# Optimization experiments

Hardware: AMD Instinct MI355X
Metric: run time of the kernel (lower is better)

Reference implementation:

```python
import jax, jax.numpy as jnp
import numpy as np

NUM_HEADS = 16
EMBED_DIM = 1024
HEAD_DIM = EMBED_DIM // NUM_HEADS  # 64


def setup_inputs() -> dict:
    key = jax.random.key(0)
    k1, k2, k3 = jax.random.split(key, 3)
    x = jax.random.normal(k1, (2, 2048, EMBED_DIM), dtype=jnp.float32)
    # torch Linear(head_dim, 3*head_dim): weight [3*hd, hd], bias [3*hd]
    # stored here as W_qkv [hd, 3*hd] so that y = x @ W_qkv + b
    lim = 1.0 / np.sqrt(HEAD_DIM)
    W_qkv = jax.random.uniform(k2, (HEAD_DIM, 3 * HEAD_DIM), minval=-lim, maxval=lim, dtype=jnp.float32)
    b_qkv = jax.random.uniform(k3, (3 * HEAD_DIM,), minval=-lim, maxval=lim, dtype=jnp.float32)
    return {"x": x, "W_qkv": W_qkv, "b_qkv": b_qkv}


def reference(x, W_qkv, b_qkv):
    B, T, E = x.shape
    # [B, T, E] -> [B, H, T, hd]
    xh = x.reshape(B, T, NUM_HEADS, HEAD_DIM).transpose(0, 2, 1, 3)
    qkv = xh @ W_qkv + b_qkv  # [B, H, T, 3*hd], shared weights across heads
    q, k, v = jnp.split(qkv, 3, axis=-1)
    scale = 1.0 / jnp.sqrt(jnp.asarray(HEAD_DIM, dtype=x.dtype))
    scores = jnp.einsum('bhqd,bhkd->bhqk', q, k) * scale  # [B, H, T, T]
    attn = jax.nn.softmax(scores, axis=-1)
    out = jnp.einsum('bhqk,bhkd->bhqd', attn, v)  # [B, H, T, hd]
    return out.transpose(0, 2, 1, 3).reshape(B, T, E)
```

## Files before the change

### kernel.cpp

```cpp
#include <hip/hip_runtime.h>
#include <hip/hip_bf16.h>

#define T_SEQ   2048
#define EMBED   1024
#define HD      64
#define NHEADS  16
#define NBH     32
#define QSCALE  0.18033688011112042f

typedef __attribute__((ext_vector_type(8))) short short8;
typedef __attribute__((ext_vector_type(4))) float f32x4;
typedef __attribute__((ext_vector_type(16))) float f32x16;
typedef __attribute__((ext_vector_type(2))) unsigned int uint2v;
typedef __attribute__((ext_vector_type(4))) unsigned int uint4v;

#if __has_builtin(__builtin_amdgcn_exp2f)
#define EXP2F __builtin_amdgcn_exp2f
#else
#define EXP2F exp2f
#endif

__device__ __forceinline__ ushort bf16r(float f) {
  union { float f; unsigned u; } v; v.f = f;
  return (ushort)((v.u + 0x8000u) >> 16);
}

__device__ __forceinline__ unsigned pk2bf_perm(float a, float b) {
  union { float f; unsigned u; } ua, ub; ua.f = a; ub.f = b;
  return __builtin_amdgcn_perm(ub.u + 0x8000u, ua.u + 0x8000u, 0x07060302u);
}
#if __has_builtin(__builtin_amdgcn_cvt_pk_bf16_f32)
typedef __attribute__((ext_vector_type(2))) __bf16 bf16x2;
__device__ __forceinline__ unsigned pkbf(float a, float b) {
  union { bf16x2 v; unsigned u; } c;
  c.v = __builtin_amdgcn_cvt_pk_bf16_f32(a, b);
  return c.u;
}
#else
#define pkbf pk2bf_perm
#endif

__device__ __forceinline__ uint2v pl32swap(unsigned a, unsigned b) {
#if __has_builtin(__builtin_amdgcn_permlane32_swap)
  return __builtin_amdgcn_permlane32_swap(a, b, false, false);
#else
  asm("v_permlane32_swap_b32 %0, %1" : "+v"(a), "+v"(b));
  return (uint2v){a, b};
#endif
}

__device__ __forceinline__ void async16(const ushort* g, ushort* l) {
  __builtin_amdgcn_global_load_lds(
      (const __attribute__((address_space(1))) unsigned int*)g,
      (__attribute__((address_space(3))) unsigned int*)l, 16, 0, 0);
}

__global__ __launch_bounds__(256) void prep_w(const float* __restrict__ W,
                                              ushort* __restrict__ Wg) {
  const int i = blockIdx.x * 256 + threadIdx.x;
  const int d = i / 192, c = i - d * 192;
  const int phys = c * 64 + (((d >> 3) ^ (c & 7)) << 3) + (d & 7);
  Wg[phys] = bf16r(W[i]);
}

__global__ __launch_bounds__(256) void qkv_proj(
    const float* __restrict__ x, const ushort* __restrict__ Wg,
    const float* __restrict__ bias,
    ushort* __restrict__ Qws, ushort* __restrict__ Kws,
    ushort* __restrict__ Vtws) {
  __shared__ ushort WtL[192 * 64];
  __shared__ __attribute__((aligned(16))) float bl[192];

  const int bx = blockIdx.x;
  const int b  = bx >> 9;
  const int h  = (bx >> 5) & 15;
  const int t0 = (bx & 31) * 64;
  const int tid = threadIdx.x;
  const int wave = tid >> 6, lane = tid & 63;
  const int quad = lane >> 4, n16 = lane & 15;

  const int trow = t0 + wave * 16 + n16;
  const float* xr = x + ((size_t)(b * T_SEQ + trow)) * EMBED + h * HD;
  short8 xa[2];
#pragma unroll
  for (int ks = 0; ks < 2; ks++) {
    f32x4 v0 = *(const f32x4*)(xr + ks * 32 + quad * 8);
    f32x4 v1 = *(const f32x4*)(xr + ks * 32 + quad * 8 + 4);
    short8 f;
    ((unsigned*)&f)[0] = pkbf(v0[0], v0[1]);
    ((unsigned*)&f)[1] = pkbf(v0[2], v0[3]);
    ((unsigned*)&f)[2] = pkbf(v1[0], v1[1]);
    ((unsigned*)&f)[3] = pkbf(v1[2], v1[3]);
    xa[ks] = f;
  }

#pragma unroll
  for (int it = 0; it < 6; it++)
    async16(Wg + it * 2048 + tid * 8, WtL + it * 2048 + wave * 512);
  if (tid < 192) bl[tid] = bias[tid];
  __syncthreads();

  const int bh = b * NHEADS + h;
  const size_t qkbase = (size_t)bh * T_SEQ * HD;
  const int tw = t0 + wave * 16;
  const int sw = n16 & 7;
  const int t = tw + n16;

#pragma unroll
  for (int nt = 0; nt < 12; nt++) {
    const ushort* wrow = WtL + (nt * 16 + n16) * 64;
    const short8 wb0 = *(short8*)(wrow + ((quad ^ sw) << 3));
    const short8 wb1 = *(short8*)(wrow + (((4 | quad) ^ sw) << 3));
    if (nt < 8) {
      f32x4 acc = (f32x4){0.f, 0.f, 0.f, 0.f};
      acc = __builtin_amdgcn_mfma_f32_16x16x32_bf16(wb0, xa[0], acc, 0, 0, 0);
      acc = __builtin_amdgcn_mfma_f32_16x16x32_bf16(wb1, xa[1], acc, 0, 0, 0);
      const f32x4 bv4 = *(const f32x4*)(bl + nt * 16 + quad * 4);
      uint2v pk;
      if (nt < 4) {
        const int d = nt * 16 + quad * 4;
        pk.x = pkbf((acc[0] + bv4[0]) * QSCALE, (acc[1] + bv4[1]) * QSCALE);
        pk.y = pkbf((acc[2] + bv4[2]) * QSCALE, (acc[3] + bv4[3]) * QSCALE);
        *(uint2v*)(Qws + qkbase + (size_t)t * HD + d) = pk;
      } else {
        const int d = (nt - 4) * 16 + quad * 4;
        pk.x = pkbf(acc[0] + bv4[0], acc[1] + bv4[1]);
        pk.y = pkbf(acc[2] + bv4[2], acc[3] + bv4[3]);
        *(uint2v*)(Kws + qkbase + (size_t)t * HD + d) = pk;
      }
    } else {
      f32x4 acc = (f32x4){0.f, 0.f, 0.f, 0.f};
      acc = __builtin_amdgcn_mfma_f32_16x16x32_bf16(xa[0], wb0, acc, 0, 0, 0);
      acc = __builtin_amdgcn_mfma_f32_16x16x32_bf16(xa[1], wb1, acc, 0, 0, 0);
      const float bv = bl[nt * 16 + n16];
      const int d = (nt - 8) * 16 + n16;
      const int tcol = tw + quad * 4;
      uint2v pk;
      pk.x = pkbf(acc[0] + bv, acc[1] + bv);
      pk.y = pkbf(acc[2] + bv, acc[3] + bv);
      *(uint2v*)(Vtws + (size_t)(bh * HD + d) * T_SEQ + tcol) = pk;
    }
  }
}

__global__ __launch_bounds__(256, 2) void flash_attn(
    const ushort* __restrict__ Qws, const ushort* __restrict__ Kws,
    const ushort* __restrict__ Vtws, float* __restrict__ out) {
  __shared__ ushort Ks[4][64 * 64];
  __shared__ ushort Vs[4][64 * 64];

  const int bx = blockIdx.x;
  const int bh = bx & 31;
  const int q0 = (bx >> 5) * 128;
  const int b = bh >> 4, h = bh & 15;
  const int tid = threadIdx.x;
  const int wave = tid >> 6, lane = tid & 63;
  const int l5 = lane & 31, H = lane >> 5, swz = lane & 7;

  const ushort* Qb = Qws + (size_t)bh * T_SEQ * HD;
  const ushort* Kb = Kws + (size_t)bh * T_SEQ * HD;
  const ushort* Vb = Vtws + (size_t)bh * HD * T_SEQ;

  short8 qb[4];
#pragma unroll
  for (int dc = 0; dc < 4; dc++)
    qb[dc] = *(const short8*)(Qb + (size_t)(q0 + wave * 32 + l5) * HD +
                              dc * 16 + H * 8);

  const int sr = tid >> 3, sp = tid & 7;
  const int sl = (sp ^ (sr & 7) ^ (((sr >> 4) & 1) << 1)) * 8;
  const ushort* pK0 = Kb + (size_t)sr * HD + sl;
  const ushort* pK1 = Kb + (size_t)(sr + 32) * HD + sl;
  const ushort* pV0 = Vb + (size_t)sr * T_SEQ + sl;
  const ushort* pV1 = Vb + (size_t)(sr + 32) * T_SEQ + sl;

  const int xr4 = ((l5 >> 4) & 1) << 1;
  int co[4];
#pragma unroll
  for (int i = 0; i < 4; i++) co[i] = ((((i << 1) | H) ^ swz ^ xr4) << 3);
  const int rbase = l5 << 6;

  short8 ones;
#pragma unroll
  for (int j = 0; j < 8; j++) ones[j] = (short)0x3F80;

  f32x16 o0, o1, lA;
#pragma unroll
  for (int i = 0; i < 16; i++) { o0[i] = 0.f; o1[i] = 0.f; lA[i] = 0.f; }

  async16(pK0, Ks[0] + wave * 512);
  async16(pK1, Ks[0] + 2048 + wave * 512);
  async16(pV0, Vs[0] + wave * 512);
  async16(pV1, Vs[0] + 2048 + wave * 512);
  async16(pK0 + 64 * HD, Ks[1] + wave * 512);
  async16(pK1 + 64 * HD, Ks[1] + 2048 + wave * 512);
  async16(pV0 + 64, Vs[1] + wave * 512);
  async16(pV1 + 64, Vs[1] + 2048 + wave * 512);
  pK0 += 128 * HD; pK1 += 128 * HD; pV0 += 128; pV1 += 128;

  for (int kt = 0; kt < 32; kt++) {
    const int cb = kt & 3;
    if (kt < 30) {
      const int pb = (kt + 2) & 3;
      async16(pK0, Ks[pb] + wave * 512);
      async16(pK1, Ks[pb] + 2048 + wave * 512);
      async16(pV0, Vs[pb] + wave * 512);
      async16(pV1, Vs[pb] + 2048 + wave * 512);
      pK0 += 64 * HD; pK1 += 64 * HD; pV0 += 64; pV1 += 64;
    }
    __builtin_amdgcn_sched_barrier(0);
    if (kt < 30)       asm volatile("s_waitcnt vmcnt(8)" ::: "memory");
    else if (kt == 30) asm volatile("s_waitcnt vmcnt(4)" ::: "memory");
    else               asm volatile("s_waitcnt vmcnt(0)" ::: "memory");
    __builtin_amdgcn_s_barrier();
    __builtin_amdgcn_sched_barrier(0);

    const ushort* Kt = Ks[cb];
    const ushort* Vt = Vs[cb];

    f32x16 s0, s1;
#pragma unroll
    for (int i = 0; i < 16; i++) { s0[i] = 0.f; s1[i] = 0.f; }
    __builtin_amdgcn_s_setprio(1);
#pragma unroll
    for (int dc = 0; dc < 4; dc++) {
      const short8 ka0 = *(short8*)(Kt + rbase + co[dc]);
      const short8 ka1 = *(short8*)(Kt + 2048 + rbase + co[dc]);
      s0 = __builtin_amdgcn_mfma_f32_32x32x16_bf16(ka0, qb[dc], s0, 0, 0, 0);
      s1 = __builtin_amdgcn_mfma_f32_32x32x16_bf16(ka1, qb[dc], s1, 0, 0, 0);
    }
    __builtin_amdgcn_s_setprio(0);

    unsigned Au[2][4], Bu[2][4];
#pragma unroll
    for (int m = 0; m < 4; m++) {
      Au[0][m] = pkbf(EXP2F(s0[4 * m]),     EXP2F(s0[4 * m + 1]));
      Bu[0][m] = pkbf(EXP2F(s0[4 * m + 2]), EXP2F(s0[4 * m + 3]));
      Au[1][m] = pkbf(EXP2F(s1[4 * m]),     EXP2F(s1[4 * m + 1]));
      Bu[1][m] = pkbf(EXP2F(s1[4 * m + 2]), EXP2F(s1[4 * m + 3]));
    }
    short8 pa[4];
#pragma unroll
    for (int kc = 0; kc < 4; kc++) {
      const int kt2 = kc >> 1, mm = (kc & 1) << 1;
      uint2v sA = pl32swap(Au[kt2][mm], Au[kt2][mm + 1]);
      uint2v sB = pl32swap(Bu[kt2][mm], Bu[kt2][mm + 1]);
      union { uint4v u; short8 s; } c;
      c.u = (uint4v){sA.x, sB.x, sA.y, sB.y};
      pa[kc] = c.s;
    }

    __builtin_amdgcn_s_setprio(1);
#pragma unroll
    for (int kc = 0; kc < 4; kc++) {
      const short8 vb0 = *(short8*)(Vt + rbase + co[kc]);
      const short8 vb1 = *(short8*)(Vt + 2048 + rbase + co[kc]);
      o0 = __builtin_amdgcn_mfma_f32_32x32x16_bf16(pa[kc], vb0, o0, 0, 0, 0);
      o1 = __builtin_amdgcn_mfma_f32_32x32x16_bf16(pa[kc], vb1, o1, 0, 0, 0);
      lA = __builtin_amdgcn_mfma_f32_32x32x16_bf16(pa[kc], ones, lA, 0, 0, 0);
    }
    __builtin_amdgcn_s_setprio(0);
  }

#pragma unroll
  for (int r = 0; r < 16; r++) {
    const int row = q0 + wave * 32 + (r & 3) + ((r >> 2) << 3) + (H << 2);
    const float rl = 1.0f / lA[r];
    float* op = out + (size_t)(b * T_SEQ + row) * EMBED + h * HD + l5;
    op[0]  = o0[r] * rl;
    op[32] = o1[r] * rl;
  }
}

extern "C" void kernel_launch(void* const* d_in, const int* in_sizes, int n_in,
                              void* d_out, int out_size, void* d_ws, size_t ws_size,
                              hipStream_t stream) {
  (void)in_sizes; (void)n_in; (void)out_size; (void)ws_size;
  const float* x    = (const float*)d_in[0];
  const float* W    = (const float*)d_in[1];
  const float* bias = (const float*)d_in[2];
  float* out = (float*)d_out;

  const size_t elems = (size_t)NBH * T_SEQ * HD;
  ushort* Qws  = (ushort*)d_ws;
  ushort* Kws  = Qws + elems;
  ushort* Vtws = Kws + elems;
  ushort* Wg   = Vtws + elems;

  prep_w<<<dim3(48), dim3(256), 0, stream>>>(W, Wg);
  qkv_proj<<<dim3(1024), dim3(256), 0, stream>>>(x, Wg, bias, Qws, Kws, Vtws);
  flash_attn<<<dim3(512), dim3(256), 0, stream>>>(Qws, Kws, Vtws, out);
}
```

Before: 125.7 us.

## Software-pipeline QK MFMA of next tile against softmax and PV of current tile

Splits the attention inner loop into a QK stage and a softmax+PV stage. It then interleaves them with two ping-pong score register sets, so the QK MFMAs for tile kt+1 are issued before the exp/pack/PV work of tile kt. The async K/V prefetch now goes out after the barrier, with a single vmcnt(4) wait per tile. The aim is to overlap VALU exp2 and packing work with matrix-core work and to shorten per-tile stalls. The cost is an extra 32 accumulator VGPRs for the second score set, which may lower occupancy or cause spills.

```diff
diff --git a/kernel.cpp b/kernel.cpp
--- a/kernel.cpp
+++ b/kernel.cpp
@@ -188,6 +188,67 @@
 #pragma unroll
   for (int i = 0; i < 16; i++) { o0[i] = 0.f; o1[i] = 0.f; lA[i] = 0.f; }
 
+  auto qk = [&](int kt, f32x16& d0, f32x16& d1) {
+    __builtin_amdgcn_sched_barrier(0);
+    if (kt < 31) asm volatile("s_waitcnt vmcnt(4)" ::: "memory");
+    else         asm volatile("s_waitcnt vmcnt(0)" ::: "memory");
+    __builtin_amdgcn_s_barrier();
+    if (kt < 30) {
+      const int pb = (kt + 2) & 3;
+      async16(pK0, Ks[pb] + wave * 512);
+      async16(pK1, Ks[pb] + 2048 + wave * 512);
+      async16(pV0, Vs[pb] + wave * 512);
+      async16(pV1, Vs[pb] + 2048 + wave * 512);
+      pK0 += 64 * HD; pK1 += 64 * HD; pV0 += 64; pV1 += 64;
+    }
+    __builtin_amdgcn_sched_barrier(0);
+
+    const ushort* Kt = Ks[kt & 3];
+#pragma unroll
+    for (int i = 0; i < 16; i++) { d0[i] = 0.f; d1[i] = 0.f; }
+    __builtin_amdgcn_s_setprio(1);
+#pragma unroll
+    for (int dc = 0; dc < 4; dc++) {
+      const short8 ka0 = *(short8*)(Kt + rbase + co[dc]);
+      const short8 ka1 = *(short8*)(Kt + 2048 + rbase + co[dc]);
+      d0 = __builtin_amdgcn_mfma_f32_32x32x16_bf16(ka0, qb[dc], d0, 0, 0, 0);
+      d1 = __builtin_amdgcn_mfma_f32_32x32x16_bf16(ka1, qb[dc], d1, 0, 0, 0);
+    }
+    __builtin_amdgcn_s_setprio(0);
+  };
+
+  auto smpv = [&](int kt, const f32x16& s0r, const f32x16& s1r) {
+    const ushort* Vt = Vs[kt & 3];
+    unsigned Au[2][4], Bu[2][4];
+#pragma unroll
+    for (int m = 0; m < 4; m++) {
+      Au[0][m] = pkbf(EXP2F(s0r[4 * m]),     EXP2F(s0r[4 * m + 1]));
+      Bu[0][m] = pkbf(EXP2F(s0r[4 * m + 2]), EXP2F(s0r[4 * m + 3]));
+      Au[1][m] = pkbf(EXP2F(s1r[4 * m]),     EXP2F(s1r[4 * m + 1]));
+      Bu[1][m] = pkbf(EXP2F(s1r[4 * m + 2]), EXP2F(s1r[4 * m + 3]));
+    }
+    short8 pa[4];
+#pragma unroll
+    for (int kc = 0; kc < 4; kc++) {
+      const int kt2 = kc >> 1, mm = (kc & 1) << 1;
+      uint2v sA = pl32swap(Au[kt2][mm], Au[kt2][mm + 1]);
+      uint2v sB = pl32swap(Bu[kt2][mm], Bu[kt2][mm + 1]);
+      union { uint4v u; short8 s; } c;
+      c.u = (uint4v){sA.x, sB.x, sA.y, sB.y};
+      pa[kc] = c.s;
+    }
+    __builtin_amdgcn_s_setprio(1);
+#pragma unroll
+    for (int kc = 0; kc < 4; kc++) {
+      const short8 vb0 = *(short8*)(Vt + rbase + co[kc]);
+      const short8 vb1 = *(short8*)(Vt + 2048 + rbase + co[kc]);
+      o0 = __builtin_amdgcn_mfma_f32_32x32x16_bf16(pa[kc], vb0, o0, 0, 0, 0);
+      o1 = __builtin_amdgcn_mfma_f32_32x32x16_bf16(pa[kc], vb1, o1, 0, 0, 0);
+      lA = __builtin_amdgcn_mfma_f32_32x32x16_bf16(pa[kc], ones, lA, 0, 0, 0);
+    }
+    __builtin_amdgcn_s_setprio(0);
+  };
+
   async16(pK0, Ks[0] + wave * 512);
   async16(pK1, Ks[0] + 2048 + wave * 512);
   async16(pV0, Vs[0] + wave * 512);
@@ -198,69 +259,17 @@
   async16(pV1 + 64, Vs[1] + 2048 + wave * 512);
   pK0 += 128 * HD; pK1 += 128 * HD; pV0 += 128; pV1 += 128;
 
-  for (int kt = 0; kt < 32; kt++) {
-    const int cb = kt & 3;
-    if (kt < 30) {
-      const int pb = (kt + 2) & 3;
-      async16(pK0, Ks[pb] + wave * 512);
-      async16(pK1, Ks[pb] + 2048 + wave * 512);
-      async16(pV0, Vs[pb] + wave * 512);
-      async16(pV1, Vs[pb] + 2048 + wave * 512);
-      pK0 += 64 * HD; pK1 += 64 * HD; pV0 += 64; pV1 += 64;
-    }
-    __builtin_amdgcn_sched_barrier(0);
-    if (kt < 30)       asm volatile("s_waitcnt vmcnt(8)" ::: "memory");
-    else if (kt == 30) asm volatile("s_waitcnt vmcnt(4)" ::: "memory");
-    else               asm volatile("s_waitcnt vmcnt(0)" ::: "memory");
-    __builtin_amdgcn_s_barrier();
-    __builtin_amdgcn_sched_barrier(0);
-
-    const ushort* Kt = Ks[cb];
-    const ushort* Vt = Vs[cb];
-
-    f32x16 s0, s1;
-#pragma unroll
-    for (int i = 0; i < 16; i++) { s0[i] = 0.f; s1[i] = 0.f; }
-    __builtin_amdgcn_s_setprio(1);
-#pragma unroll
-    for (int dc = 0; dc < 4; dc++) {
-      const short8 ka0 = *(short8*)(Kt + rbase + co[dc]);
-      const short8 ka1 = *(short8*)(Kt + 2048 + rbase + co[dc]);
-      s0 = __builtin_amdgcn_mfma_f32_32x32x16_bf16(ka0, qb[dc], s0, 0, 0, 0);
-      s1 = __builtin_amdgcn_mfma_f32_32x32x16_bf16(ka1, qb[dc], s1, 0, 0, 0);
-    }
-    __builtin_amdgcn_s_setprio(0);
-
-    unsigned Au[2][4], Bu[2][4];
-#pragma unroll
-    for (int m = 0; m < 4; m++) {
-      Au[0][m] = pkbf(EXP2F(s0[4 * m]),     EXP2F(s0[4 * m + 1]));
-      Bu[0][m] = pkbf(EXP2F(s0[4 * m + 2]), EXP2F(s0[4 * m + 3]));
-      Au[1][m] = pkbf(EXP2F(s1[4 * m]),     EXP2F(s1[4 * m + 1]));
-      Bu[1][m] = pkbf(EXP2F(s1[4 * m + 2]), EXP2F(s1[4 * m + 3]));
-    }
-    short8 pa[4];
-#pragma unroll
-    for (int kc = 0; kc < 4; kc++) {
-      const int kt2 = kc >> 1, mm = (kc & 1) << 1;
-      uint2v sA = pl32swap(Au[kt2][mm], Au[kt2][mm + 1]);
-      uint2v sB = pl32swap(Bu[kt2][mm], Bu[kt2][mm + 1]);
-      union { uint4v u; short8 s; } c;
-      c.u = (uint4v){sA.x, sB.x, sA.y, sB.y};
-      pa[kc] = c.s;
-    }
-
-    __builtin_amdgcn_s_setprio(1);
-#pragma unroll
-    for (int kc = 0; kc < 4; kc++) {
-      const short8 vb0 = *(short8*)(Vt + rbase + co[kc]);
-      const short8 vb1 = *(short8*)(Vt + 2048 + rbase + co[kc]);
-      o0 = __builtin_amdgcn_mfma_f32_32x32x16_bf16(pa[kc], vb0, o0, 0, 0, 0);
-      o1 = __builtin_amdgcn_mfma_f32_32x32x16_bf16(pa[kc], vb1, o1, 0, 0, 0);
-      lA = __builtin_amdgcn_mfma_f32_32x32x16_bf16(pa[kc], ones, lA, 0, 0, 0);
-    }
-    __builtin_amdgcn_s_setprio(0);
+  f32x16 sA0, sA1, sB0, sB1;
+  qk(0, sA0, sA1);
+  for (int kt = 1; kt < 31; kt += 2) {
+    qk(kt, sB0, sB1);
+    smpv(kt - 1, sA0, sA1);
+    qk(kt + 1, sA0, sA1);
+    smpv(kt, sB0, sB1);
   }
+  qk(31, sB0, sB1);
+  smpv(30, sA0, sA1);
+  smpv(31, sB0, sB1);
 
 #pragma unroll
   for (int r = 0; r < 16; r++) {
```

Result: no change. 125.3 us (-0.3%).

## Split key range across two wave groups per block and merge partials via LDS

Applied to the files above, without the earlier changes.

Doubles the flash-attention block to 512 threads: two groups of four waves each process half of the key sequence for the same 128 query rows. Each group uses its own double-buffered K/V LDS region, replacing the previous four-deep prefetch ring. At the end the second group writes its partial O and row-sum accumulators to LDS, and the first group adds them before normalizing and storing. The aim is more resident waves per CU to hide latency, at the cost of a shallower prefetch pipeline, a final reduction step, and a launch bound of 512 threads with 4 blocks that may force register spilling.

```diff
diff --git a/kernel.cpp b/kernel.cpp
--- a/kernel.cpp
+++ b/kernel.cpp
@@ -143,11 +143,11 @@
   }
 }
 
-__global__ __launch_bounds__(256, 2) void flash_attn(
+__global__ __launch_bounds__(512, 4) void flash_attn(
     const ushort* __restrict__ Qws, const ushort* __restrict__ Kws,
     const ushort* __restrict__ Vtws, float* __restrict__ out) {
-  __shared__ ushort Ks[4][64 * 64];
-  __shared__ ushort Vs[4][64 * 64];
+  __shared__ ushort Ks[2][2][64 * 64];
+  __shared__ ushort Vs[2][2][64 * 64];
 
   const int bx = blockIdx.x;
   const int bh = bx & 31;
@@ -155,24 +155,35 @@
   const int b = bh >> 4, h = bh & 15;
   const int tid = threadIdx.x;
   const int wave = tid >> 6, lane = tid & 63;
+  const int half = wave >> 2, wsub = wave & 3;
   const int l5 = lane & 31, H = lane >> 5, swz = lane & 7;
 
   const ushort* Qb = Qws + (size_t)bh * T_SEQ * HD;
   const ushort* Kb = Kws + (size_t)bh * T_SEQ * HD;
   const ushort* Vb = Vtws + (size_t)bh * HD * T_SEQ;
 
+  ushort* KsH = &Ks[half][0][0];
+  ushort* VsH = &Vs[half][0][0];
+
+  const int hid = tid & 255;
+  const int sr = hid >> 3, sp = hid & 7;
+  const int sl = (sp ^ (sr & 7) ^ (((sr >> 4) & 1) << 1)) * 8;
+  const ushort* pK0 = Kb + (size_t)(half * 1024 + sr) * HD + sl;
+  const ushort* pK1 = Kb + (size_t)(half * 1024 + sr + 32) * HD + sl;
+  const ushort* pV0 = Vb + (size_t)sr * T_SEQ + half * 1024 + sl;
+  const ushort* pV1 = Vb + (size_t)(sr + 32) * T_SEQ + half * 1024 + sl;
+
+  async16(pK0, KsH + wsub * 512);
+  async16(pK1, KsH + 2048 + wsub * 512);
+  async16(pV0, VsH + wsub * 512);
+  async16(pV1, VsH + 2048 + wsub * 512);
+  pK0 += 64 * HD; pK1 += 64 * HD; pV0 += 64; pV1 += 64;
+
   short8 qb[4];
 #pragma unroll
   for (int dc = 0; dc < 4; dc++)
-    qb[dc] = *(const short8*)(Qb + (size_t)(q0 + wave * 32 + l5) * HD +
+    qb[dc] = *(const short8*)(Qb + (size_t)(q0 + wsub * 32 + l5) * HD +
                               dc * 16 + H * 8);
-
-  const int sr = tid >> 3, sp = tid & 7;
-  const int sl = (sp ^ (sr & 7) ^ (((sr >> 4) & 1) << 1)) * 8;
-  const ushort* pK0 = Kb + (size_t)sr * HD + sl;
-  const ushort* pK1 = Kb + (size_t)(sr + 32) * HD + sl;
-  const ushort* pV0 = Vb + (size_t)sr * T_SEQ + sl;
-  const ushort* pV1 = Vb + (size_t)(sr + 32) * T_SEQ + sl;
 
   const int xr4 = ((l5 >> 4) & 1) << 1;
   int co[4];
@@ -188,35 +199,22 @@
 #pragma unroll
   for (int i = 0; i < 16; i++) { o0[i] = 0.f; o1[i] = 0.f; lA[i] = 0.f; }
 
-  async16(pK0, Ks[0] + wave * 512);
-  async16(pK1, Ks[0] + 2048 + wave * 512);
-  async16(pV0, Vs[0] + wave * 512);
-  async16(pV1, Vs[0] + 2048 + wave * 512);
-  async16(pK0 + 64 * HD, Ks[1] + wave * 512);
-  async16(pK1 + 64 * HD, Ks[1] + 2048 + wave * 512);
-  async16(pV0 + 64, Vs[1] + wave * 512);
-  async16(pV1 + 64, Vs[1] + 2048 + wave * 512);
-  pK0 += 128 * HD; pK1 += 128 * HD; pV0 += 128; pV1 += 128;
-
-  for (int kt = 0; kt < 32; kt++) {
-    const int cb = kt & 3;
-    if (kt < 30) {
-      const int pb = (kt + 2) & 3;
-      async16(pK0, Ks[pb] + wave * 512);
-      async16(pK1, Ks[pb] + 2048 + wave * 512);
-      async16(pV0, Vs[pb] + wave * 512);
-      async16(pV1, Vs[pb] + 2048 + wave * 512);
+  for (int j = 0; j < 16; j++) {
+    __builtin_amdgcn_sched_barrier(0);
+    asm volatile("s_waitcnt vmcnt(0)" ::: "memory");
+    __builtin_amdgcn_s_barrier();
+    if (j < 15) {
+      const int pb = (j + 1) & 1;
+      async16(pK0, KsH + pb * 4096 + wsub * 512);
+      async16(pK1, KsH + pb * 4096 + 2048 + wsub * 512);
+      async16(pV0, VsH + pb * 4096 + wsub * 512);
+      async16(pV1, VsH + pb * 4096 + 2048 + wsub * 512);
       pK0 += 64 * HD; pK1 += 64 * HD; pV0 += 64; pV1 += 64;
     }
     __builtin_amdgcn_sched_barrier(0);
-    if (kt < 30)       asm volatile("s_waitcnt vmcnt(8)" ::: "memory");
-    else if (kt == 30) asm volatile("s_waitcnt vmcnt(4)" ::: "memory");
-    else               asm volatile("s_waitcnt vmcnt(0)" ::: "memory");
-    __builtin_amdgcn_s_barrier();
-    __builtin_amdgcn_sched_barrier(0);
-
-    const ushort* Kt = Ks[cb];
-    const ushort* Vt = Vs[cb];
+
+    const ushort* Kt = KsH + (j & 1) * 4096;
+    const ushort* Vt = VsH + (j & 1) * 4096;
 
     f32x16 s0, s1;
 #pragma unroll
@@ -262,13 +260,29 @@
     __builtin_amdgcn_s_setprio(0);
   }
 
-#pragma unroll
-  for (int r = 0; r < 16; r++) {
-    const int row = q0 + wave * 32 + (r & 3) + ((r >> 2) << 3) + (H << 2);
-    const float rl = 1.0f / lA[r];
-    float* op = out + (size_t)(b * T_SEQ + row) * EMBED + h * HD + l5;
-    op[0]  = o0[r] * rl;
-    op[32] = o1[r] * rl;
+  __syncthreads();
+  float* LF = (wsub < 2) ? ((float*)&Ks[0][0][0]) + wsub * 3072
+                         : ((float*)&Vs[0][0][0]) + (wsub - 2) * 3072;
+  if (half == 1) {
+    float* myb = LF + lane * 48;
+    *(f32x16*)(myb)      = o0;
+    *(f32x16*)(myb + 16) = o1;
+    *(f32x16*)(myb + 32) = lA;
+  }
+  __syncthreads();
+  if (half == 0) {
+    const float* pb = LF + lane * 48;
+    const f32x16 b0 = *(const f32x16*)(pb);
+    const f32x16 b1 = *(const f32x16*)(pb + 16);
+    const f32x16 b2 = *(const f32x16*)(pb + 32);
+#pragma unroll
+    for (int r = 0; r < 16; r++) {
+      const int row = q0 + wsub * 32 + (r & 3) + ((r >> 2) << 3) + (H << 2);
+      const float rl = 1.0f / (lA[r] + b2[r]);
+      float* op = out + (size_t)(b * T_SEQ + row) * EMBED + h * HD + l5;
+      op[0]  = (o0[r] + b0[r]) * rl;
+      op[32] = (o1[r] + b1[r]) * rl;
+    }
   }
 }
 
@@ -289,5 +303,5 @@
 
   prep_w<<<dim3(48), dim3(256), 0, stream>>>(W, Wg);
   qkv_proj<<<dim3(1024), dim3(256), 0, stream>>>(x, Wg, bias, Qws, Kws, Vtws);
-  flash_attn<<<dim3(512), dim3(256), 0, stream>>>(Qws, Kws, Vtws, out);
-}
+  flash_attn<<<dim3(512), dim3(512), 0, stream>>>(Qws, Kws, Vtws, out);
+}
```

Result: no change. 125.4 us (-0.3%).
